# Optimization experiments

Measured on AMD Instinct MI355X. Metric: run time of the kernel, lower is better.

## Reference

```python
import jax, jax.numpy as jnp
import numpy as np

B_SZ, N_IN, N_CTX, UNITS, RANK = 4096, 4096, 512, 4096, 256


def setup_inputs() -> dict:
    key = jax.random.key(0)
    ks = jax.random.split(key, 8)
    inputs = jax.random.normal(ks[0], (B_SZ, N_IN), dtype=jnp.float32)
    context = jax.random.normal(ks[1], (B_SZ, N_CTX), dtype=jnp.float32)
    # Orthogonal-ish init approximated by scaled normals (math-equivalent shapes)
    U = jax.random.normal(ks[2], (N_IN, RANK), dtype=jnp.float32) / np.sqrt(N_IN)
    S = jax.random.uniform(ks[3], (RANK,), dtype=jnp.float32, minval=0.5, maxval=1.5)
    V = jax.random.normal(ks[4], (UNITS, RANK), dtype=jnp.float32) / np.sqrt(UNITS)
    W = jax.random.normal(ks[5], (N_CTX, RANK), dtype=jnp.float32) / np.sqrt(N_CTX)
    B = jnp.zeros((RANK,), dtype=jnp.float32)
    bias = jnp.zeros((UNITS,), dtype=jnp.float32)
    return {"inputs": inputs, "context": context, "U": U, "S": S, "V": V, "W": W, "B": B, "bias": bias}


def reference(inputs, context, U, S, V, W, B, bias):
    # chi[b,r] = sigmoid(context @ W + B)
    chi = jax.nn.sigmoid(context @ W + B)                  # [B, R]
    # Original: kernel[b,n,m] = sum_r U[n,r]*S[r]*chi[b,r]*V[m,r];
    # out[b,m] = sum_n x[b,n]*kernel[b,n,m]. Algebraically equal to:
    t = (inputs @ U) * (S * chi)                           # [B, R]
    out = t @ V.T + bias                                   # first '+ self.bias'
    out = out + bias                                       # 'outputs += self.bias' (use_bias=True)
    return jax.nn.relu(out)
```

## Files before the change

### kernel.cpp

```cpp
#include <hip/hip_runtime.h>

#define B_SZ 4096
#define N_IN 4096
#define N_CTX 512
#define UNITS 4096
#define RANK 256
#define ZSPLIT 16

typedef __attribute__((ext_vector_type(8))) __bf16 bf16x8;
typedef __attribute__((ext_vector_type(4))) float f32x4;
typedef __attribute__((ext_vector_type(8))) unsigned short ushort8;

__device__ __forceinline__ unsigned short f2bf(float f) {
    __bf16 h = (__bf16)f;
    return __builtin_bit_cast(unsigned short, h);
}
__device__ __forceinline__ float bf2f(unsigned short h) {
    return __uint_as_float(((unsigned int)h) << 16);
}
__device__ __forceinline__ void gload_lds16(const unsigned short* g, unsigned short* l) {
    __builtin_amdgcn_global_load_lds(
        (const __attribute__((address_space(1))) unsigned int*)g,
        (__attribute__((address_space(3))) unsigned int*)l, 16, 0, 0);
}
__device__ __forceinline__ bf16x8 ldfrag(const unsigned short* p) {
    ushort8 t = *(const ushort8*)p;
    return __builtin_bit_cast(bf16x8, t);
}

__global__ void prep(const float* __restrict__ U, const float* __restrict__ W,
                     const float* __restrict__ V,
                     unsigned short* __restrict__ UT, unsigned short* __restrict__ WT,
                     unsigned short* __restrict__ Vb) {
    __shared__ unsigned short t[64][66];
    int bid = blockIdx.x, tid = threadIdx.x;
    if (bid < 288) {
        const float* src; unsigned short* dst; int R, C, rb, cb;
        if (bid < 256) { src = U; dst = UT; R = N_IN; C = RANK; rb = (bid & 63) * 64; cb = (bid >> 6) * 64; }
        else { int b = bid - 256; src = W; dst = WT; R = N_CTX; C = RANK; rb = (b & 7) * 64; cb = (b >> 3) * 64; }
        int r = tid >> 4, c4 = (tid & 15) * 4;
        for (int i = 0; i < 4; i++) {
            float4 v = *(const float4*)(src + (size_t)(rb + r + i * 16) * C + cb + c4);
            t[r + i * 16][c4 + 0] = f2bf(v.x);
            t[r + i * 16][c4 + 1] = f2bf(v.y);
            t[r + i * 16][c4 + 2] = f2bf(v.z);
            t[r + i * 16][c4 + 3] = f2bf(v.w);
        }
        __syncthreads();
        int c = tid >> 3, r8 = (tid & 7) * 8;
        for (int j = 0; j < 2; j++) {
            int cc = c + j * 32;
            ushort8 o;
            for (int k = 0; k < 8; k++) o[k] = t[r8 + k][cc];
            *(ushort8*)(dst + (size_t)(cb + cc) * R + rb + r8) = o;
        }
    } else {
        size_t base = (size_t)(bid - 288) * 2048 + (size_t)tid * 8;
        float4 a = *(const float4*)(V + base);
        float4 b = *(const float4*)(V + base + 4);
        ushort8 o = { f2bf(a.x), f2bf(a.y), f2bf(a.z), f2bf(a.w),
                      f2bf(b.x), f2bf(b.y), f2bf(b.z), f2bf(b.w) };
        *(ushort8*)(Vb + base) = o;
    }
}


__launch_bounds__(256, 4)
__global__ void k1_chi(const float* __restrict__ ctx, const unsigned short* __restrict__ WT,
                       const float* __restrict__ S, const float* __restrict__ Bb,
                       unsigned short* __restrict__ Schi) {
    __shared__ unsigned short As[32 * 64];
    __shared__ unsigned short Bs[64 * 64];
    int tid = threadIdx.x, w = tid >> 6, lane = tid & 63;
    int ln15 = lane & 15, quad = lane >> 4;
    int wr = w >> 1, wc = w & 1;
    int tm = blockIdx.y * 32, tn = blockIdx.x * 64;
    f32x4 acc2[2] = {};
    int arow = tid >> 3, acs = tid & 7;
    const float* ag = ctx + (size_t)(tm + arow) * N_CTX + acs * 8;
    unsigned short* al = As + arow * 64 + (acs ^ (arow & 7)) * 8;
    int bl8 = lane >> 3, bcs = lane & 7;
    int bgc = (bcs ^ bl8) * 8;
    for (int kt = 0; kt < 8; kt++) {
        int k0 = kt * 64;
        for (int c = 0; c < 2; c++) {
            int row = w * 16 + c * 8 + bl8;
            gload_lds16(WT + (size_t)(tn + row) * N_CTX + k0 + bgc, Bs + row * 64 + bcs * 8);
        }
        {
            float4 v0 = *(const float4*)(ag + k0);
            float4 v1 = *(const float4*)(ag + k0 + 4);
            ushort8 a8 = { f2bf(v0.x), f2bf(v0.y), f2bf(v0.z), f2bf(v0.w),
                           f2bf(v1.x), f2bf(v1.y), f2bf(v1.z), f2bf(v1.w) };
            *(ushort8*)al = a8;
        }
        __syncthreads();
        for (int kh = 0; kh < 2; kh++) {
            int ch = kh * 4 + quad;
            bf16x8 af = ldfrag(As + (wr * 16 + ln15) * 64 + (ch ^ (ln15 & 7)) * 8);
            for (int j = 0; j < 2; j++) {
                int row = wc * 32 + j * 16 + ln15;
                bf16x8 bfr = ldfrag(Bs + row * 64 + (ch ^ (ln15 & 7)) * 8);
                acc2[j] = __builtin_amdgcn_mfma_f32_16x16x32_bf16(af, bfr, acc2[j], 0, 0, 0);
            }
        }
        __syncthreads();
    }
    for (int j = 0; j < 2; j++) {
        int col = tn + wc * 32 + j * 16 + ln15;
        float sv = S[col], bv = Bb[col];
        for (int r = 0; r < 4; r++) {
            int row = tm + wr * 16 + quad * 4 + r;
            float x = acc2[j][r] + bv;
            float chi = sv / (1.f + __expf(-x));
            Schi[(size_t)row * RANK + col] = f2bf(chi);
        }
    }
}

__launch_bounds__(512, 2)
__global__ void k2_t0(const float* __restrict__ X, const unsigned short* __restrict__ UT,
                      unsigned short* __restrict__ T0p) {
    __shared__ char smem[49152];
    unsigned short* As = (unsigned short*)smem;
    unsigned short* Bs = As + 128 * 64;
    int tid = threadIdx.x, w = tid >> 6, lane = tid & 63;
    int ln15 = lane & 15, quad = lane >> 4;
    int wr = w >> 2, wc = w & 3;
    int tm = blockIdx.y * 128;
    int kbase = blockIdx.z * (N_IN / ZSPLIT);
    f32x4 acc[4][4] = {};
    int arow = tid >> 2, acs0 = (tid & 3) * 2;
    const float* ag = X + (size_t)(tm + arow) * N_IN + kbase + acs0 * 8;
    unsigned short* al0 = As + arow * 64 + ((acs0 + 0) ^ (arow & 7)) * 8;
    unsigned short* al1 = As + arow * 64 + ((acs0 + 1) ^ (arow & 7)) * 8;
    int bl8 = lane >> 3, bcs = lane & 7;
    int bgc = (bcs ^ bl8) * 8;
    for (int kt = 0; kt < (N_IN / ZSPLIT) / 64; kt++) {
        int k0 = kt * 64;
        for (int c = 0; c < 4; c++) {
            int row = w * 32 + c * 8 + bl8;
            gload_lds16(UT + (size_t)row * N_IN + kbase + k0 + bgc, Bs + row * 64 + bcs * 8);
        }
        {
            float4 v0 = *(const float4*)(ag + k0);
            float4 v1 = *(const float4*)(ag + k0 + 4);
            float4 u0 = *(const float4*)(ag + k0 + 8);
            float4 u1 = *(const float4*)(ag + k0 + 12);
            ushort8 a8 = { f2bf(v0.x), f2bf(v0.y), f2bf(v0.z), f2bf(v0.w),
                           f2bf(v1.x), f2bf(v1.y), f2bf(v1.z), f2bf(v1.w) };
            ushort8 b8 = { f2bf(u0.x), f2bf(u0.y), f2bf(u0.z), f2bf(u0.w),
                           f2bf(u1.x), f2bf(u1.y), f2bf(u1.z), f2bf(u1.w) };
            *(ushort8*)al0 = a8;
            *(ushort8*)al1 = b8;
        }
        __syncthreads();
        for (int kh = 0; kh < 2; kh++) {
            int ch = kh * 4 + quad;
            int sw = (ch ^ (ln15 & 7)) * 8;
            bf16x8 af[4];
            for (int i = 0; i < 4; i++)
                af[i] = ldfrag(As + (wr * 64 + i * 16 + ln15) * 64 + sw);
            for (int j = 0; j < 4; j++) {
                bf16x8 b = ldfrag(Bs + (wc * 64 + j * 16 + ln15) * 64 + sw);
                for (int i = 0; i < 4; i++)
                    acc[i][j] = __builtin_amdgcn_mfma_f32_16x16x32_bf16(af[i], b, acc[i][j], 0, 0, 0);
            }
        }
        __syncthreads();
    }
    unsigned short* P = T0p + (size_t)blockIdx.z * B_SZ * RANK;
    unsigned short* ep = (unsigned short*)smem;
    const int EPW = 280;
    int er = tid >> 3, ec0 = tid & 7;
    for (int h = 0; h < 2; h++) {
        if (wr == h) {
            for (int i = 0; i < 4; i++)
                for (int j = 0; j < 4; j++)
                    for (int r = 0; r < 4; r++)
                        ep[(i * 16 + quad * 4 + r) * EPW + wc * 64 + j * 16 + ln15] = f2bf(acc[i][j][r]);
        }
        __syncthreads();
        for (int k = 0; k < 4; k++) {
            int chunk = ec0 + 8 * k;
            *(ushort8*)(P + (size_t)(tm + h * 64 + er) * RANK + chunk * 8) =
                *(const ushort8*)(ep + er * EPW + chunk * 8);
        }
        __syncthreads();
    }
}

__global__ void e_red(const unsigned short* __restrict__ T0p, const unsigned short* __restrict__ Schi,
                      unsigned short* __restrict__ T) {
    int i = blockIdx.x * 256 + threadIdx.x;
    const size_t stride = (size_t)B_SZ * RANK;
    float a[8] = {};
    for (int z = 0; z < ZSPLIT; z++) {
        ushort8 p = *(const ushort8*)(T0p + z * stride + (size_t)i * 8);
        for (int k = 0; k < 8; k++) a[k] += bf2f(p[k]);
    }
    ushort8 s = *(const ushort8*)(Schi + (size_t)i * 8);
    ushort8 o;
    for (int k = 0; k < 8; k++) o[k] = f2bf(a[k] * bf2f(s[k]));
    *(ushort8*)(T + (size_t)i * 8) = o;
}

__launch_bounds__(256, 3)
__global__ void k3_out(const unsigned short* __restrict__ T, const unsigned short* __restrict__ Vb,
                       const float* __restrict__ bias, float* __restrict__ out) {
    __shared__ char smem[34816];
    unsigned short* As = (unsigned short*)smem;
    unsigned short* Bs = As + 128 * 64;
    int tid = threadIdx.x, w = tid >> 6, lane = tid & 63;
    int ln15 = lane & 15, quad = lane >> 4;
    int wr = w >> 1, wc = w & 1;
    int tn = blockIdx.x * 128, tm = blockIdx.y * 128;
    f32x4 acc[4][4] = {};
    int bl8 = lane >> 3, bcs = lane & 7;
    int bgc = (bcs ^ bl8) * 8;
    for (int kt = 0; kt < RANK / 64; kt++) {
        int k0 = kt * 64;
        for (int c = 0; c < 4; c++) {
            int row = w * 32 + c * 8 + bl8;
            gload_lds16(T + (size_t)(tm + row) * RANK + k0 + bgc, As + row * 64 + bcs * 8);
            gload_lds16(Vb + (size_t)(tn + row) * RANK + k0 + bgc, Bs + row * 64 + bcs * 8);
        }
        __syncthreads();
        for (int kh = 0; kh < 2; kh++) {
            int ch = kh * 4 + quad;
            int sw = (ch ^ (ln15 & 7)) * 8;
            bf16x8 af[4], bfr[4];
            for (int i = 0; i < 4; i++)
                af[i] = ldfrag(As + (wr * 64 + i * 16 + ln15) * 64 + sw);
            for (int j = 0; j < 4; j++)
                bfr[j] = ldfrag(Bs + (wc * 64 + j * 16 + ln15) * 64 + sw);
            for (int i = 0; i < 4; i++)
                for (int j = 0; j < 4; j++)
                    acc[i][j] = __builtin_amdgcn_mfma_f32_16x16x32_bf16(af[i], bfr[j], acc[i][j], 0, 0, 0);
        }
        __syncthreads();
    }
    float* ep = (float*)smem;
    const int EPW = 136;
    int er = tid >> 2, ec0 = tid & 3;
    for (int h = 0; h < 2; h++) {
        if (wr == h) {
            for (int j = 0; j < 4; j++) {
                int col = wc * 64 + j * 16 + ln15;
                float bv = 2.f * bias[tn + col];
                for (int i = 0; i < 4; i++)
                    for (int r = 0; r < 4; r++)
                        ep[(i * 16 + quad * 4 + r) * EPW + col] = fmaxf(acc[i][j][r] + bv, 0.f);
            }
        }
        __syncthreads();
        for (int k = 0; k < 8; k++) {
            int chunk = ec0 + 4 * k;
            *(float4*)(out + (size_t)(tm + h * 64 + er) * UNITS + tn + chunk * 4) =
                *(const float4*)(ep + er * EPW + chunk * 4);
        }
        __syncthreads();
    }
}

extern "C" void kernel_launch(void* const* d_in, const int* in_sizes, int n_in,
                              void* d_out, int out_size, void* d_ws, size_t ws_size,
                              hipStream_t stream) {
    (void)in_sizes; (void)n_in; (void)out_size; (void)ws_size;
    const float* inputs  = (const float*)d_in[0];
    const float* context = (const float*)d_in[1];
    const float* U       = (const float*)d_in[2];
    const float* S       = (const float*)d_in[3];
    const float* V       = (const float*)d_in[4];
    const float* W       = (const float*)d_in[5];
    const float* Bb      = (const float*)d_in[6];
    const float* bias    = (const float*)d_in[7];
    float* out = (float*)d_out;

    char* ws = (char*)d_ws;
    size_t o = 0;
    unsigned short* UT   = (unsigned short*)(ws + o); o += (size_t)RANK * N_IN * 2;
    unsigned short* WT   = (unsigned short*)(ws + o); o += (size_t)RANK * N_CTX * 2;
    unsigned short* Vb   = (unsigned short*)(ws + o); o += (size_t)UNITS * RANK * 2;
    unsigned short* Schi = (unsigned short*)(ws + o); o += (size_t)B_SZ * RANK * 2;
    unsigned short* T    = (unsigned short*)(ws + o); o += (size_t)B_SZ * RANK * 2;
    unsigned short* T0p  = (unsigned short*)(ws + o); o += (size_t)ZSPLIT * B_SZ * RANK * 2;

    prep<<<800, 256, 0, stream>>>(U, W, V, UT, WT, Vb);
    k2_t0<<<dim3(1, B_SZ / 128, ZSPLIT), 512, 0, stream>>>(inputs, UT, T0p);
    k1_chi<<<dim3(RANK / 64, B_SZ / 32), 256, 0, stream>>>(context, WT, S, Bb, Schi);
    e_red<<<(B_SZ * RANK) / (256 * 8), 256, 0, stream>>>(T0p, Schi, T);
    k3_out<<<dim3(UNITS / 128, B_SZ / 128), 256, 0, stream>>>(T, Vb, bias, out);
}
```

Before: 175.4 us.

## Merge chi and T0 GEMMs into one launch and widen output GEMM tiles

Combines the context GEMM (chi) and the split-K inputs@U GEMM into a single kernel that dispatches on block index. The chi work is packed two sub-blocks per 512-thread block so both run concurrently and one launch is saved. The final output GEMM moves to 128x256 tiles with 512 threads, which loads each T tile once per wider column span but uses more LDS per block and may reduce occupancy.

Result: no change. 175.0 us (-0.2%).

```diff
diff --git a/kernel.cpp b/kernel.cpp
--- a/kernel.cpp
+++ b/kernel.cpp
@@ -65,94 +65,175 @@
 }
 
 
-__launch_bounds__(256, 4)
-__global__ void k1_chi(const float* __restrict__ ctx, const unsigned short* __restrict__ WT,
-                       const float* __restrict__ S, const float* __restrict__ Bb,
-                       unsigned short* __restrict__ Schi) {
-    __shared__ unsigned short As[32 * 64];
-    __shared__ unsigned short Bs[64 * 64];
-    int tid = threadIdx.x, w = tid >> 6, lane = tid & 63;
+__launch_bounds__(512, 2)
+__global__ void k21(const float* __restrict__ X, const unsigned short* __restrict__ UT,
+                    unsigned short* __restrict__ T0p,
+                    const float* __restrict__ ctx, const unsigned short* __restrict__ WT,
+                    const float* __restrict__ S, const float* __restrict__ Bb,
+                    unsigned short* __restrict__ Schi) {
+    __shared__ char smem[49152];
+    int tid = threadIdx.x, bfull = blockIdx.x;
+    int w = tid >> 6, lane = tid & 63;
     int ln15 = lane & 15, quad = lane >> 4;
-    int wr = w >> 1, wc = w & 1;
-    int tm = blockIdx.y * 32, tn = blockIdx.x * 64;
-    f32x4 acc2[2] = {};
-    int arow = tid >> 3, acs = tid & 7;
-    const float* ag = ctx + (size_t)(tm + arow) * N_CTX + acs * 8;
-    unsigned short* al = As + arow * 64 + (acs ^ (arow & 7)) * 8;
-    int bl8 = lane >> 3, bcs = lane & 7;
-    int bgc = (bcs ^ bl8) * 8;
-    for (int kt = 0; kt < 8; kt++) {
-        int k0 = kt * 64;
-        for (int c = 0; c < 2; c++) {
-            int row = w * 16 + c * 8 + bl8;
-            gload_lds16(WT + (size_t)(tn + row) * N_CTX + k0 + bgc, Bs + row * 64 + bcs * 8);
-        }
-        {
-            float4 v0 = *(const float4*)(ag + k0);
-            float4 v1 = *(const float4*)(ag + k0 + 4);
-            ushort8 a8 = { f2bf(v0.x), f2bf(v0.y), f2bf(v0.z), f2bf(v0.w),
-                           f2bf(v1.x), f2bf(v1.y), f2bf(v1.z), f2bf(v1.w) };
-            *(ushort8*)al = a8;
-        }
-        __syncthreads();
-        for (int kh = 0; kh < 2; kh++) {
-            int ch = kh * 4 + quad;
-            bf16x8 af = ldfrag(As + (wr * 16 + ln15) * 64 + (ch ^ (ln15 & 7)) * 8);
-            for (int j = 0; j < 2; j++) {
-                int row = wc * 32 + j * 16 + ln15;
-                bf16x8 bfr = ldfrag(Bs + row * 64 + (ch ^ (ln15 & 7)) * 8);
-                acc2[j] = __builtin_amdgcn_mfma_f32_16x16x32_bf16(af, bfr, acc2[j], 0, 0, 0);
-            }
-        }
-        __syncthreads();
-    }
-    for (int j = 0; j < 2; j++) {
-        int col = tn + wc * 32 + j * 16 + ln15;
-        float sv = S[col], bv = Bb[col];
-        for (int r = 0; r < 4; r++) {
-            int row = tm + wr * 16 + quad * 4 + r;
-            float x = acc2[j][r] + bv;
-            float chi = sv / (1.f + __expf(-x));
-            Schi[(size_t)row * RANK + col] = f2bf(chi);
-        }
-    }
+    if (bfull < 512) {
+        int z = bfull >> 5, my = bfull & 31;
+        unsigned short* As = (unsigned short*)smem;
+        unsigned short* Bs = As + 128 * 64;
+        int wr = w >> 2, wc = w & 3;
+        int tm = my * 128;
+        int kbase = z * (N_IN / ZSPLIT);
+        f32x4 acc[4][4] = {};
+        int arow = tid >> 2, acs0 = (tid & 3) * 2;
+        const float* ag = X + (size_t)(tm + arow) * N_IN + kbase + acs0 * 8;
+        unsigned short* al0 = As + arow * 64 + ((acs0 + 0) ^ (arow & 7)) * 8;
+        unsigned short* al1 = As + arow * 64 + ((acs0 + 1) ^ (arow & 7)) * 8;
+        int bl8 = lane >> 3, bcs = lane & 7;
+        int bgc = (bcs ^ bl8) * 8;
+        for (int kt = 0; kt < (N_IN / ZSPLIT) / 64; kt++) {
+            int k0 = kt * 64;
+            for (int c = 0; c < 4; c++) {
+                int row = w * 32 + c * 8 + bl8;
+                gload_lds16(UT + (size_t)row * N_IN + kbase + k0 + bgc, Bs + row * 64 + bcs * 8);
+            }
+            {
+                float4 v0 = *(const float4*)(ag + k0);
+                float4 v1 = *(const float4*)(ag + k0 + 4);
+                float4 u0 = *(const float4*)(ag + k0 + 8);
+                float4 u1 = *(const float4*)(ag + k0 + 12);
+                ushort8 a8 = { f2bf(v0.x), f2bf(v0.y), f2bf(v0.z), f2bf(v0.w),
+                               f2bf(v1.x), f2bf(v1.y), f2bf(v1.z), f2bf(v1.w) };
+                ushort8 b8 = { f2bf(u0.x), f2bf(u0.y), f2bf(u0.z), f2bf(u0.w),
+                               f2bf(u1.x), f2bf(u1.y), f2bf(u1.z), f2bf(u1.w) };
+                *(ushort8*)al0 = a8;
+                *(ushort8*)al1 = b8;
+            }
+            __syncthreads();
+            for (int kh = 0; kh < 2; kh++) {
+                int ch = kh * 4 + quad;
+                int sw = (ch ^ (ln15 & 7)) * 8;
+                bf16x8 af[4];
+                for (int i = 0; i < 4; i++)
+                    af[i] = ldfrag(As + (wr * 64 + i * 16 + ln15) * 64 + sw);
+                for (int j = 0; j < 4; j++) {
+                    bf16x8 b = ldfrag(Bs + (wc * 64 + j * 16 + ln15) * 64 + sw);
+                    for (int i = 0; i < 4; i++)
+                        acc[i][j] = __builtin_amdgcn_mfma_f32_16x16x32_bf16(af[i], b, acc[i][j], 0, 0, 0);
+                }
+            }
+            __syncthreads();
+        }
+        unsigned short* P = T0p + (size_t)z * B_SZ * RANK;
+        unsigned short* ep = (unsigned short*)smem;
+        const int EPW = 280;
+        int er = tid >> 3, ec0 = tid & 7;
+        for (int h = 0; h < 2; h++) {
+            if (wr == h) {
+                for (int i = 0; i < 4; i++)
+                    for (int j = 0; j < 4; j++)
+                        for (int r = 0; r < 4; r++)
+                            ep[(i * 16 + quad * 4 + r) * EPW + wc * 64 + j * 16 + ln15] = f2bf(acc[i][j][r]);
+            }
+            __syncthreads();
+            for (int k = 0; k < 4; k++) {
+                int chunk = ec0 + 8 * k;
+                *(ushort8*)(P + (size_t)(tm + h * 64 + er) * RANK + chunk * 8) =
+                    *(const ushort8*)(ep + er * EPW + chunk * 8);
+            }
+            __syncthreads();
+        }
+    } else {
+        int hh = tid >> 8;
+        int sb = (bfull - 512) * 2 + hh;
+        int bx = sb & 3, by = sb >> 2;
+        int t = tid & 255;
+        int lw = t >> 6, llane = t & 63;
+        int lln15 = llane & 15, lquad = llane >> 4;
+        int wr = lw >> 1, wc = lw & 1;
+        unsigned short* base = (unsigned short*)smem + hh * 6144;
+        unsigned short* As = base;
+        unsigned short* Bs = base + 32 * 64;
+        int tm = by * 32, tn = bx * 64;
+        f32x4 acc2[2] = {};
+        int arow = t >> 3, acs = t & 7;
+        const float* ag = ctx + (size_t)(tm + arow) * N_CTX + acs * 8;
+        unsigned short* al = As + arow * 64 + (acs ^ (arow & 7)) * 8;
+        int bl8 = llane >> 3, bcs = llane & 7;
+        int bgc = (bcs ^ bl8) * 8;
+        for (int kt = 0; kt < 8; kt++) {
+            int k0 = kt * 64;
+            for (int c = 0; c < 2; c++) {
+                int row = lw * 16 + c * 8 + bl8;
+                gload_lds16(WT + (size_t)(tn + row) * N_CTX + k0 + bgc, Bs + row * 64 + bcs * 8);
+            }
+            {
+                float4 v0 = *(const float4*)(ag + k0);
+                float4 v1 = *(const float4*)(ag + k0 + 4);
+                ushort8 a8 = { f2bf(v0.x), f2bf(v0.y), f2bf(v0.z), f2bf(v0.w),
+                               f2bf(v1.x), f2bf(v1.y), f2bf(v1.z), f2bf(v1.w) };
+                *(ushort8*)al = a8;
+            }
+            __syncthreads();
+            for (int kh = 0; kh < 2; kh++) {
+                int ch = kh * 4 + lquad;
+                bf16x8 af = ldfrag(As + (wr * 16 + lln15) * 64 + (ch ^ (lln15 & 7)) * 8);
+                for (int j = 0; j < 2; j++) {
+                    int row = wc * 32 + j * 16 + lln15;
+                    bf16x8 bfr = ldfrag(Bs + row * 64 + (ch ^ (lln15 & 7)) * 8);
+                    acc2[j] = __builtin_amdgcn_mfma_f32_16x16x32_bf16(af, bfr, acc2[j], 0, 0, 0);
+                }
+            }
+            __syncthreads();
+        }
+        for (int j = 0; j < 2; j++) {
+            int col = tn + wc * 32 + j * 16 + lln15;
+            float sv = S[col], bv = Bb[col];
+            for (int r = 0; r < 4; r++) {
+                int row = tm + wr * 16 + lquad * 4 + r;
+                float x = acc2[j][r] + bv;
+                float chi = sv / (1.f + __expf(-x));
+                Schi[(size_t)row * RANK + col] = f2bf(chi);
+            }
+        }
+    }
+}
+
+__global__ void e_red(const unsigned short* __restrict__ T0p, const unsigned short* __restrict__ Schi,
+                      unsigned short* __restrict__ T) {
+    int i = blockIdx.x * 256 + threadIdx.x;
+    const size_t stride = (size_t)B_SZ * RANK;
+    float a[8] = {};
+    for (int z = 0; z < ZSPLIT; z++) {
+        ushort8 p = *(const ushort8*)(T0p + z * stride + (size_t)i * 8);
+        for (int k = 0; k < 8; k++) a[k] += bf2f(p[k]);
+    }
+    ushort8 s = *(const ushort8*)(Schi + (size_t)i * 8);
+    ushort8 o;
+    for (int k = 0; k < 8; k++) o[k] = f2bf(a[k] * bf2f(s[k]));
+    *(ushort8*)(T + (size_t)i * 8) = o;
 }
 
 __launch_bounds__(512, 2)
-__global__ void k2_t0(const float* __restrict__ X, const unsigned short* __restrict__ UT,
-                      unsigned short* __restrict__ T0p) {
-    __shared__ char smem[49152];
+__global__ void k3_out(const unsigned short* __restrict__ T, const unsigned short* __restrict__ Vb,
+                       const float* __restrict__ bias, float* __restrict__ out) {
+    __shared__ char smem[66560];
     unsigned short* As = (unsigned short*)smem;
     unsigned short* Bs = As + 128 * 64;
     int tid = threadIdx.x, w = tid >> 6, lane = tid & 63;
     int ln15 = lane & 15, quad = lane >> 4;
     int wr = w >> 2, wc = w & 3;
-    int tm = blockIdx.y * 128;
-    int kbase = blockIdx.z * (N_IN / ZSPLIT);
+    int tn = blockIdx.x * 256, tm = blockIdx.y * 128;
     f32x4 acc[4][4] = {};
-    int arow = tid >> 2, acs0 = (tid & 3) * 2;
-    const float* ag = X + (size_t)(tm + arow) * N_IN + kbase + acs0 * 8;
-    unsigned short* al0 = As + arow * 64 + ((acs0 + 0) ^ (arow & 7)) * 8;
-    unsigned short* al1 = As + arow * 64 + ((acs0 + 1) ^ (arow & 7)) * 8;
     int bl8 = lane >> 3, bcs = lane & 7;
     int bgc = (bcs ^ bl8) * 8;
-    for (int kt = 0; kt < (N_IN / ZSPLIT) / 64; kt++) {
+    for (int kt = 0; kt < RANK / 64; kt++) {
         int k0 = kt * 64;
+        for (int c = 0; c < 2; c++) {
+            int row = w * 16 + c * 8 + bl8;
+            gload_lds16(T + (size_t)(tm + row) * RANK + k0 + bgc, As + row * 64 + bcs * 8);
+        }
         for (int c = 0; c < 4; c++) {
             int row = w * 32 + c * 8 + bl8;
-            gload_lds16(UT + (size_t)row * N_IN + kbase + k0 + bgc, Bs + row * 64 + bcs * 8);
-        }
-        {
-            float4 v0 = *(const float4*)(ag + k0);
-            float4 v1 = *(const float4*)(ag + k0 + 4);
-            float4 u0 = *(const float4*)(ag + k0 + 8);
-            float4 u1 = *(const float4*)(ag + k0 + 12);
-            ushort8 a8 = { f2bf(v0.x), f2bf(v0.y), f2bf(v0.z), f2bf(v0.w),
-                           f2bf(v1.x), f2bf(v1.y), f2bf(v1.z), f2bf(v1.w) };
-            ushort8 b8 = { f2bf(u0.x), f2bf(u0.y), f2bf(u0.z), f2bf(u0.w),
-                           f2bf(u1.x), f2bf(u1.y), f2bf(u1.z), f2bf(u1.w) };
-            *(ushort8*)al0 = a8;
-            *(ushort8*)al1 = b8;
+            gload_lds16(Vb + (size_t)(tn + row) * RANK + k0 + bgc, Bs + row * 64 + bcs * 8);
         }
         __syncthreads();
         for (int kh = 0; kh < 2; kh++) {
@@ -169,80 +250,9 @@
         }
         __syncthreads();
     }
-    unsigned short* P = T0p + (size_t)blockIdx.z * B_SZ * RANK;
-    unsigned short* ep = (unsigned short*)smem;
-    const int EPW = 280;
+    float* ep = (float*)smem;
+    const int EPW = 260;
     int er = tid >> 3, ec0 = tid & 7;
-    for (int h = 0; h < 2; h++) {
-        if (wr == h) {
-            for (int i = 0; i < 4; i++)
-                for (int j = 0; j < 4; j++)
-                    for (int r = 0; r < 4; r++)
-                        ep[(i * 16 + quad * 4 + r) * EPW + wc * 64 + j * 16 + ln15] = f2bf(acc[i][j][r]);
-        }
-        __syncthreads();
-        for (int k = 0; k < 4; k++) {
-            int chunk = ec0 + 8 * k;
-            *(ushort8*)(P + (size_t)(tm + h * 64 + er) * RANK + chunk * 8) =
-                *(const ushort8*)(ep + er * EPW + chunk * 8);
-        }
-        __syncthreads();
-    }
-}
-
-__global__ void e_red(const unsigned short* __restrict__ T0p, const unsigned short* __restrict__ Schi,
-                      unsigned short* __restrict__ T) {
-    int i = blockIdx.x * 256 + threadIdx.x;
-    const size_t stride = (size_t)B_SZ * RANK;
-    float a[8] = {};
-    for (int z = 0; z < ZSPLIT; z++) {
-        ushort8 p = *(const ushort8*)(T0p + z * stride + (size_t)i * 8);
-        for (int k = 0; k < 8; k++) a[k] += bf2f(p[k]);
-    }
-    ushort8 s = *(const ushort8*)(Schi + (size_t)i * 8);
-    ushort8 o;
-    for (int k = 0; k < 8; k++) o[k] = f2bf(a[k] * bf2f(s[k]));
-    *(ushort8*)(T + (size_t)i * 8) = o;
-}
-
-__launch_bounds__(256, 3)
-__global__ void k3_out(const unsigned short* __restrict__ T, const unsigned short* __restrict__ Vb,
-                       const float* __restrict__ bias, float* __restrict__ out) {
-    __shared__ char smem[34816];
-    unsigned short* As = (unsigned short*)smem;
-    unsigned short* Bs = As + 128 * 64;
-    int tid = threadIdx.x, w = tid >> 6, lane = tid & 63;
-    int ln15 = lane & 15, quad = lane >> 4;
-    int wr = w >> 1, wc = w & 1;
-    int tn = blockIdx.x * 128, tm = blockIdx.y * 128;
-    f32x4 acc[4][4] = {};
-    int bl8 = lane >> 3, bcs = lane & 7;
-    int bgc = (bcs ^ bl8) * 8;
-    for (int kt = 0; kt < RANK / 64; kt++) {
-        int k0 = kt * 64;
-        for (int c = 0; c < 4; c++) {
-            int row = w * 32 + c * 8 + bl8;
-            gload_lds16(T + (size_t)(tm + row) * RANK + k0 + bgc, As + row * 64 + bcs * 8);
-            gload_lds16(Vb + (size_t)(tn + row) * RANK + k0 + bgc, Bs + row * 64 + bcs * 8);
-        }
-        __syncthreads();
-        for (int kh = 0; kh < 2; kh++) {
-            int ch = kh * 4 + quad;
-            int sw = (ch ^ (ln15 & 7)) * 8;
-            bf16x8 af[4], bfr[4];
-            for (int i = 0; i < 4; i++)
-                af[i] = ldfrag(As + (wr * 64 + i * 16 + ln15) * 64 + sw);
-            for (int j = 0; j < 4; j++)
-                bfr[j] = ldfrag(Bs + (wc * 64 + j * 16 + ln15) * 64 + sw);
-            for (int i = 0; i < 4; i++)
-                for (int j = 0; j < 4; j++)
-                    acc[i][j] = __builtin_amdgcn_mfma_f32_16x16x32_bf16(af[i], bfr[j], acc[i][j], 0, 0, 0);
-        }
-        __syncthreads();
-    }
-    float* ep = (float*)smem;
-    const int EPW = 136;
-    int er = tid >> 2, ec0 = tid & 3;
     for (int h = 0; h < 2; h++) {
         if (wr == h) {
             for (int j = 0; j < 4; j++) {
@@ -255,7 +265,7 @@
         }
         __syncthreads();
         for (int k = 0; k < 8; k++) {
-            int chunk = ec0 + 4 * k;
+            int chunk = ec0 + 8 * k;
             *(float4*)(out + (size_t)(tm + h * 64 + er) * UNITS + tn + chunk * 4) =
                 *(const float4*)(ep + er * EPW + chunk * 4);
         }
@@ -287,8 +297,7 @@
     unsigned short* T0p  = (unsigned short*)(ws + o); o += (size_t)ZSPLIT * B_SZ * RANK * 2;
 
     prep<<<800, 256, 0, stream>>>(U, W, V, UT, WT, Vb);
-    k2_t0<<<dim3(1, B_SZ / 128, ZSPLIT), 512, 0, stream>>>(inputs, UT, T0p);
-    k1_chi<<<dim3(RANK / 64, B_SZ / 32), 256, 0, stream>>>(context, WT, S, Bb, Schi);
+    k21<<<768, 512, 0, stream>>>(inputs, UT, T0p, context, WT, S, Bb, Schi);
     e_red<<<(B_SZ * RANK) / (256 * 8), 256, 0, stream>>>(T0p, Schi, T);
-    k3_out<<<dim3(UNITS / 128, B_SZ / 128), 256, 0, stream>>>(T, Vb, bias, out);
-}
+    k3_out<<<dim3(UNITS / 256, B_SZ / 128), 512, 0, stream>>>(T, Vb, bias, out);
+}
```
